# Performance work log

Hardware: AMD Instinct MI355X
Metric: run time of the kernel (lower is better)

## Reference

```python
import jax, jax.numpy as jnp
import numpy as np

B, S, HID = 2, 2048, 2048
H, K, D = 32, 8, 64          # query heads, kv heads, head_dim
G = H // K                   # GQA group size
ROPE_MSCALE = 1.2            # constant rope_mscale applied to q and k
SM_SCALE = 1.0 / (D ** 0.5)  # flash_attn default softmax scale


def rotate_half(x):
    h = x.shape[-1] // 2
    return jnp.concatenate([-x[..., h:], x[..., :h]], axis=-1)


def setup_inputs() -> dict:
    key = jax.random.key(0)
    k1, k2, k3, k4 = jax.random.split(key, 4)
    hidden_states = jax.random.normal(k1, (B, S, HID), dtype=jnp.float32)
    # standard rotary tables: cos/sin of shape [S, D]
    inv_freq = 1.0 / (10000.0 ** (jnp.arange(0, D, 2, dtype=jnp.float32) / D))
    freqs = jnp.outer(jnp.arange(S, dtype=jnp.float32), inv_freq)  # [S, D/2]
    emb = jnp.concatenate([freqs, freqs], axis=-1)                 # [S, D]
    cos, sin = jnp.cos(emb), jnp.sin(emb)
    per_head_scale = 1.0 + 0.1 * jax.random.normal(k2, (B, H), dtype=jnp.float32)
    Wqkv = jax.random.normal(k3, ((H + 2 * K) * D, HID), dtype=jnp.float32) * (HID ** -0.5)
    Wo = jax.random.normal(k4, (HID, H * D), dtype=jnp.float32) * ((H * D) ** -0.5)
    return {"cos": cos, "sin": sin, "hidden_states": hidden_states,
            "per_head_scale": per_head_scale, "Wqkv": Wqkv, "Wo": Wo}


def reference(cos, sin, hidden_states, per_head_scale, Wqkv, Wo):
    # fused QKV projection (CastedLinear, no bias)
    qkv = jnp.einsum('bsh,oh->bso', hidden_states, Wqkv)          # [B,S,(H+2K)*D]
    qkv = qkv.reshape(B, S, H + 2 * K, D)
    q = qkv[:, :, :H]                 # [B,S,H,D]
    k = qkv[:, :, H:H + K]            # [B,S,K,D]
    v = qkv[:, :, H + K:]             # [B,S,K,D]
    # rotary embedding: cos/sin [S,D] -> broadcast over heads via [S,1,D]
    c = cos[:, None, :]
    s_ = sin[:, None, :]
    q = q * c + rotate_half(q) * s_
    k = k * c + rotate_half(k) * s_
    # rope_mscale
    q = q * ROPE_MSCALE
    k = k * ROPE_MSCALE
    # per-head scale on queries: [B,H] -> [B,1,H,1]
    q = q * per_head_scale[:, None, :, None]
    # GQA attention without materializing repeated K/V: group query heads
    qg = q.reshape(B, S, K, G, D)
    scores = jnp.einsum('bqkgd,bskd->bkgqs', qg, k) * SM_SCALE    # [B,K,G,Sq,Sk]
    causal = jnp.arange(S)[:, None] >= jnp.arange(S)[None, :]     # [Sq,Sk]
    scores = jnp.where(causal, scores, jnp.finfo(scores.dtype).min)
    probs = jax.nn.softmax(scores, axis=-1)
    out = jnp.einsum('bkgqs,bskd->bqkgd', probs, v).reshape(B, S, H * D)
    return jnp.einsum('bso,ho->bsh', out, Wo)                     # o_proj
```

## Files before the change

kernel.cpp:

```cpp
#include <hip/hip_runtime.h>
#include <stdint.h>

typedef unsigned short u16;
typedef short short8 __attribute__((ext_vector_type(8)));
typedef float f32x4 __attribute__((ext_vector_type(4)));
typedef uint32_t u32x4 __attribute__((ext_vector_type(4)));

#define S_LEN 2048
#define NQH 32
#define NKH 8
#define DHD 64
#define MNEG -1.0e30f

__device__ __forceinline__ float b2f(u16 u){
  union { uint32_t i; float f; } c; c.i = ((uint32_t)u) << 16; return c.f;
}
__device__ __forceinline__ u16 f2b(float f){
  union { float f; uint32_t i; } c; c.f = f;
  uint32_t r = c.i + 0x7fffu + ((c.i >> 16) & 1u);
  return (u16)(r >> 16);
}
__device__ __forceinline__ uint32_t cvt_pk_bf16(float lo, float hi){
  uint32_t r;
  asm("v_cvt_pk_bf16_f32 %0, %1, %2" : "=v"(r) : "v"(lo), "v"(hi));
  return r;
}
__device__ __forceinline__ void gload_lds16(const void* g, void* l){
  __builtin_amdgcn_global_load_lds((const __attribute__((address_space(1))) uint32_t*)g,
                                   (__attribute__((address_space(3))) uint32_t*)l, 16, 0, 0);
}

__global__ __launch_bounds__(256) void cvt_all(const float* __restrict__ hs,
                                               const float* __restrict__ wq,
                                               const float* __restrict__ wo,
                                               u16* __restrict__ hsB,
                                               u16* __restrict__ wqB,
                                               u16* __restrict__ woB){
  int i = blockIdx.x * 256 + threadIdx.x;
  const float* src; u16* dst; int off;
  if (i < 2097152)      { src = hs; dst = hsB; off = i; }
  else if (i < 3670016) { src = wq; dst = wqB; off = i - 2097152; }
  else                  { src = wo; dst = woB; off = i - 3670016; }
  float4 v = ((const float4*)src)[off];
  uint2 o;
  o.x = (uint32_t)f2b(v.x) | ((uint32_t)f2b(v.y) << 16);
  o.y = (uint32_t)f2b(v.z) | ((uint32_t)f2b(v.w) << 16);
  ((uint2*)dst)[off] = o;
}

template<int OUT_F32>
__global__ __launch_bounds__(256)
void gemm_bt(const u16* __restrict__ A, const u16* __restrict__ Bm,
             void* __restrict__ Cp, int N, int K)
{
  __shared__ alignas(16) u16 lA[128 * 64];
  __shared__ alignas(16) u16 lB[128 * 64];
  const int tid = threadIdx.x;
  const int w = tid >> 6, l = tid & 63;
  const int lg = l >> 4, lc = l & 15;
  const int wm = w >> 1, wn = w & 1;
  const int m0 = blockIdx.y * 128, n0 = blockIdx.x * 128;
  const int srow = l >> 3, sc = l & 7;
  const size_t ldb = (size_t)K * 2;
  f32x4 acc[4][4] = {};
  const int kiters = K >> 6;
  for (int kt = 0; kt < kiters; ++kt){
    __syncthreads();
#pragma unroll
    for (int i = 0; i < 4; ++i){
      const int row = (i * 4 + w) * 8 + srow;
      const int gc = ((sc ^ (row & 7)) << 4);
      gload_lds16((const char*)A + (size_t)(m0 + row) * ldb + (size_t)kt * 128 + gc,
                  (char*)lA + row * 128 + sc * 16);
    }
#pragma unroll
    for (int i = 0; i < 4; ++i){
      const int row = (i * 4 + w) * 8 + srow;
      const int gc = ((sc ^ (row & 7)) << 4);
      gload_lds16((const char*)Bm + (size_t)(n0 + row) * ldb + (size_t)kt * 128 + gc,
                  (char*)lB + row * 128 + sc * 16);
    }
    __syncthreads();
#pragma unroll
    for (int kk = 0; kk < 2; ++kk){
      short8 af[4], bfr[4];
#pragma unroll
      for (int mi = 0; mi < 4; ++mi){
        const int row = wm * 64 + mi * 16 + lc;
        const int cc = (kk * 4 + lg) ^ (row & 7);
        af[mi] = *(const short8*)((const char*)lA + row * 128 + cc * 16);
      }
#pragma unroll
      for (int ni = 0; ni < 4; ++ni){
        const int row = wn * 64 + ni * 16 + lc;
        const int cc = (kk * 4 + lg) ^ (row & 7);
        bfr[ni] = *(const short8*)((const char*)lB + row * 128 + cc * 16);
      }
#pragma unroll
      for (int mi = 0; mi < 4; ++mi)
#pragma unroll
        for (int ni = 0; ni < 4; ++ni)
          acc[mi][ni] = __builtin_amdgcn_mfma_f32_16x16x32_bf16(af[mi], bfr[ni], acc[mi][ni], 0, 0, 0);
    }
  }
  const int r0 = m0 + wm * 64 + lg * 4;
  const int c0 = n0 + wn * 64 + lc;
#pragma unroll
  for (int mi = 0; mi < 4; ++mi)
#pragma unroll
    for (int ni = 0; ni < 4; ++ni)
#pragma unroll
      for (int j = 0; j < 4; ++j){
        const size_t idx = (size_t)(r0 + mi * 16 + j) * (size_t)N + (size_t)(c0 + ni * 16);
        if (OUT_F32) ((float*)Cp)[idx] = acc[mi][ni][j];
        else         ((u16*)Cp)[idx]  = f2b(acc[mi][ni][j]);
      }
}

__global__ __launch_bounds__(256)
void rope_kernel(const u16* __restrict__ qkv, const float* __restrict__ cosT,
                 const float* __restrict__ sinT, const float* __restrict__ phs,
                 u16* __restrict__ Qo, u16* __restrict__ Ko)
{
  int id = blockIdx.x * 256 + threadIdx.x;
  int b = (id >= 327680) ? 1 : 0;
  int rem = id - b * 327680;
  int head = rem >> 13;
  int s = (rem >> 2) & 2047;
  int d0 = (rem & 3) << 4;
  const u16* src = qkv + (((size_t)(b * S_LEN + s) * 48 + head) << 6);
  uint4 xa = *(const uint4*)(src + d0);
  uint4 xb = *(const uint4*)(src + d0 + 8);
  int d0p = (d0 + 32) & 63;
  uint4 pa = *(const uint4*)(src + d0p);
  uint4 pb = *(const uint4*)(src + d0p + 8);
  const float* cp = cosT + s * 64 + d0;
  const float* sp = sinT + s * 64 + d0;
  const float sgn = (d0 < 32) ? -1.f : 1.f;
  const float kscale = 0.18033688011112042f;
  const float scale = (head < NQH) ? 1.2f * kscale * phs[b * NQH + head] : 1.2f;
  uint32_t xs[4] = {xa.x, xa.y, xa.z, xa.w};
  uint32_t xs2[4] = {xb.x, xb.y, xb.z, xb.w};
  uint32_t ps[4] = {pa.x, pa.y, pa.z, pa.w};
  uint32_t ps2[4] = {pb.x, pb.y, pb.z, pb.w};
  uint32_t ow[8];
#pragma unroll
  for (int k = 0; k < 4; ++k){
    float v0 = b2f((u16)(xs[k] & 0xffff)) * cp[2*k]   + sgn * b2f((u16)(ps[k] & 0xffff)) * sp[2*k];
    float v1 = b2f((u16)(xs[k] >> 16))    * cp[2*k+1] + sgn * b2f((u16)(ps[k] >> 16))    * sp[2*k+1];
    ow[k] = (uint32_t)f2b(v0 * scale) | ((uint32_t)f2b(v1 * scale) << 16);
  }
#pragma unroll
  for (int k = 0; k < 4; ++k){
    float v0 = b2f((u16)(xs2[k] & 0xffff)) * cp[8+2*k]   + sgn * b2f((u16)(ps2[k] & 0xffff)) * sp[8+2*k];
    float v1 = b2f((u16)(xs2[k] >> 16))    * cp[8+2*k+1] + sgn * b2f((u16)(ps2[k] >> 16))    * sp[8+2*k+1];
    ow[4+k] = (uint32_t)f2b(v0 * scale) | ((uint32_t)f2b(v1 * scale) << 16);
  }
  u16* dst;
  if (head < NQH) dst = Qo + (((size_t)(b * NQH + head) * S_LEN + s) << 6) + d0;
  else            dst = Ko + (((size_t)(b * NKH + head - NQH) * S_LEN + s) << 6) + d0;
  uint4 o0 = {ow[0], ow[1], ow[2], ow[3]};
  uint4 o1 = {ow[4], ow[5], ow[6], ow[7]};
  *(uint4*)dst = o0;
  *(uint4*)(dst + 8) = o1;
}

__global__ __launch_bounds__(256)
void vtrans(const u16* __restrict__ qkv, u16* __restrict__ VT)
{
  int bid = blockIdx.x;
  int t = bid & 15, kh = (bid >> 4) & 7, b = bid >> 7;
  __shared__ u16 vlds[128][72];
  int tid = threadIdx.x;
  {
    int r = tid >> 1, half = tid & 1;
    const u16* src = qkv + (((size_t)(b * S_LEN + t * 128 + r) * 48 + 40 + kh) << 6) + half * 32;
    uint4 a0 = *(const uint4*)(src);
    uint4 a1 = *(const uint4*)(src + 8);
    uint4 a2 = *(const uint4*)(src + 16);
    uint4 a3 = *(const uint4*)(src + 24);
    *(uint4*)&vlds[r][half * 32]      = a0;
    *(uint4*)&vlds[r][half * 32 + 8]  = a1;
    *(uint4*)&vlds[r][half * 32 + 16] = a2;
    *(uint4*)&vlds[r][half * 32 + 24] = a3;
  }
  __syncthreads();
  const int d = tid >> 2, kk2 = tid & 3;
  u16* dst = VT + ((size_t)(b * NKH + kh) * 64 + d) * S_LEN + t * 128 + kk2 * 32;
#pragma unroll
  for (int j = 0; j < 4; ++j){
    u16 o[8];
#pragma unroll
    for (int e = 0; e < 8; ++e){
      const int hk = kk2 * 32 + ((e >> 2) << 4) + j * 4 + (e & 3);
      o[e] = vlds[hk][d];
    }
    uint4 ov = { (uint32_t)o[0] | ((uint32_t)o[1] << 16), (uint32_t)o[2] | ((uint32_t)o[3] << 16),
                 (uint32_t)o[4] | ((uint32_t)o[5] << 16), (uint32_t)o[6] | ((uint32_t)o[7] << 16) };
    *(uint4*)(dst + j * 8) = ov;
  }
}

__device__ __forceinline__ void proc_chunk(f32x4 (&sv)[8], float& mrow, float& lsum,
                                           f32x4 (&o)[4], uint32_t (&pw)[4][4],
                                           const int lg, const int lc,
                                           const bool diag, const int qloc)
{
  if (diag){
#pragma unroll
    for (int nj = 0; nj < 8; ++nj)
#pragma unroll
      for (int jj = 0; jj < 4; ++jj){
        const int kloc = nj * 16 + lg * 4 + jj;
        if (kloc > qloc) sv[nj][jj] = MNEG;
      }
  }
  float mu = sv[0][0];
#pragma unroll
  for (int nj = 0; nj < 8; ++nj)
#pragma unroll
    for (int jj = 0; jj < 4; ++jj) mu = fmaxf(mu, sv[nj][jj]);
  mu = fmaxf(mu, __shfl_xor(mu, 16));
  mu = fmaxf(mu, __shfl_xor(mu, 32));
  if (!__all(mu <= mrow + 11.54f)){
    const float mnew = fmaxf(mrow, mu);
    const float sf = __builtin_amdgcn_exp2f(mrow - mnew);
    mrow = mnew;
    lsum *= sf;
#pragma unroll
    for (int dn = 0; dn < 4; ++dn)
#pragma unroll
      for (int jj = 0; jj < 4; ++jj) o[dn][jj] *= sf;
  }
  const float mcur = mrow;
  float ps = 0.f;
#pragma unroll
  for (int nj = 0; nj < 8; ++nj)
#pragma unroll
    for (int jj = 0; jj < 4; ++jj){
      const float pv = __builtin_amdgcn_exp2f(sv[nj][jj] - mcur);
      sv[nj][jj] = pv;
      ps += pv;
    }
  lsum += ps;
#pragma unroll
  for (int kk2 = 0; kk2 < 4; ++kk2){
    pw[kk2][0] = cvt_pk_bf16(sv[kk2 * 2][0],     sv[kk2 * 2][1]);
    pw[kk2][1] = cvt_pk_bf16(sv[kk2 * 2][2],     sv[kk2 * 2][3]);
    pw[kk2][2] = cvt_pk_bf16(sv[kk2 * 2 + 1][0], sv[kk2 * 2 + 1][1]);
    pw[kk2][3] = cvt_pk_bf16(sv[kk2 * 2 + 1][2], sv[kk2 * 2 + 1][3]);
  }
}

__device__ __forceinline__ short8 pw_frag(const uint32_t* pw){
  u32x4 v = { pw[0], pw[1], pw[2], pw[3] };
  return __builtin_bit_cast(short8, v);
}

__global__ __launch_bounds__(512, 2)
void attn_kernel(const u16* __restrict__ Q, const u16* __restrict__ Kr,
                 const u16* __restrict__ VT, u16* __restrict__ Ao)
{
  int bid = blockIdx.x;
  int p  = bid & 15;
  int gp = (bid >> 4) & 1;
  int kh = (bid >> 5) & 7;
  int b  = bid >> 8;
  const int qt0 = p, qt1 = 31 - p;

  __shared__ alignas(16) u16 lK[2][128 * 64];
  __shared__ alignas(16) u16 lV[2][64 * 128];

  const int tid = threadIdx.x;
  const int hh = tid >> 8;
  const int h  = kh * 4 + gp * 2 + hh;
  const int w  = (tid >> 6) & 3;
  const int l  = tid & 63;
  const int lg = l >> 4, lc = l & 15;

  short8 qf[2][2];
  {
    const u16* qbase = Q + ((size_t)(b * NQH + h) * S_LEN) * 64;
#pragma unroll
    for (int kk = 0; kk < 2; ++kk){
      qf[0][kk] = *(const short8*)(qbase + (size_t)(qt0 * 64 + w * 16 + lc) * 64 + kk * 32 + lg * 8);
      qf[1][kk] = *(const short8*)(qbase + (size_t)(qt1 * 64 + w * 16 + lc) * 64 + kk * 32 + lg * 8);
    }
  }

  const u16* Kb = Kr + (size_t)(b * NKH + kh) * S_LEN * 64;
  const u16* Vb = VT + (size_t)(b * NKH + kh) * 64 * S_LEN;

  f32x4 o[2][4] = {};
  float mrow[2] = {MNEG, MNEG};
  float lsum[2] = {0.f, 0.f};

  const int nt = (qt1 >> 1) + 1;
  const int nt0 = qt0 >> 1;

#define STAGE(T, BSEL) do { \
    _Pragma("unroll") \
    for (int i_ = 0; i_ < 2; ++i_){ \
      const int row_ = i_ * 64 + (tid >> 3); \
      const int ch_  = tid & 7; \
      const int gc_  = ((ch_ ^ (row_ & 7)) << 4); \
      gload_lds16((const char*)(Kb + (size_t)((T) * 128 + row_) * 64) + gc_, \
                  (char*)lK[BSEL] + row_ * 128 + ch_ * 16); \
    } \
    _Pragma("unroll") \
    for (int i_ = 0; i_ < 2; ++i_){ \
      const int row_ = i_ * 32 + (tid >> 4); \
      const int ch_  = tid & 15; \
      const int gc_  = ((ch_ ^ (row_ & 15)) << 4); \
      gload_lds16((const char*)(Vb + (size_t)row_ * S_LEN + (T) * 128) + gc_, \
                  (char*)lV[BSEL] + row_ * 256 + ch_ * 16); \
    } \
  } while (0)

  STAGE(0, 0);

  for (int t = 0; t < nt; ++t){
    const int cur = t & 1;
    const bool act0 = (t <= nt0);
    if (t + 1 < nt){
      STAGE(t + 1, cur ^ 1);
      asm volatile("s_waitcnt vmcnt(4)" ::: "memory");
    } else {
      asm volatile("s_waitcnt vmcnt(0)" ::: "memory");
    }
    __builtin_amdgcn_s_barrier();

    f32x4 sv[2][8] = {};
    __builtin_amdgcn_s_setprio(1);
#pragma unroll
    for (int kk = 0; kk < 2; ++kk){
      short8 kf[8];
#pragma unroll
      for (int nj = 0; nj < 8; ++nj){
        const int row = nj * 16 + lc;
        const int cc = (kk * 4 + lg) ^ (row & 7);
        kf[nj] = *(const short8*)((const char*)lK[cur] + row * 128 + cc * 16);
      }
      if (act0)
#pragma unroll
        for (int nj = 0; nj < 8; ++nj)
          sv[0][nj] = __builtin_amdgcn_mfma_f32_16x16x32_bf16(kf[nj], qf[0][kk], sv[0][nj], 0, 0, 0);
#pragma unroll
      for (int nj = 0; nj < 8; ++nj)
        sv[1][nj] = __builtin_amdgcn_mfma_f32_16x16x32_bf16(kf[nj], qf[1][kk], sv[1][nj], 0, 0, 0);
    }
    __builtin_amdgcn_s_setprio(0);

    uint32_t pw[2][4][4];
    if (act0)
      proc_chunk(sv[0], mrow[0], lsum[0], o[0], pw[0], lg, lc,
                 t == (qt0 >> 1), (qt0 & 1) * 64 + w * 16 + lc);
    proc_chunk(sv[1], mrow[1], lsum[1], o[1], pw[1], lg, lc,
               t == (qt1 >> 1), (qt1 & 1) * 64 + w * 16 + lc);

    __builtin_amdgcn_s_setprio(1);
#pragma unroll
    for (int kk2 = 0; kk2 < 4; ++kk2){
      short8 vf[4];
#pragma unroll
      for (int dn = 0; dn < 4; ++dn){
        const int row = dn * 16 + lc;
        const int cc = (kk2 * 4 + lg) ^ (row & 15);
        vf[dn] = *(const short8*)((const char*)lV[cur] + row * 256 + cc * 16);
      }
      if (act0){
        const short8 pb0 = pw_frag(pw[0][kk2]);
#pragma unroll
        for (int dn = 0; dn < 4; ++dn)
          o[0][dn] = __builtin_amdgcn_mfma_f32_16x16x32_bf16(vf[dn], pb0, o[0][dn], 0, 0, 0);
      }
      const short8 pb1 = pw_frag(pw[1][kk2]);
#pragma unroll
      for (int dn = 0; dn < 4; ++dn)
        o[1][dn] = __builtin_amdgcn_mfma_f32_16x16x32_bf16(vf[dn], pb1, o[1][dn], 0, 0, 0);
    }
    __builtin_amdgcn_s_setprio(0);
    __builtin_amdgcn_s_barrier();
  }
#undef STAGE

#pragma unroll
  for (int c = 0; c < 2; ++c){
    const int qt = c ? qt1 : qt0;
    float ls = lsum[c];
    ls += __shfl_xor(ls, 16);
    ls += __shfl_xor(ls, 32);
    const float inv = 1.f / ls;
    const int sq = qt * 64 + w * 16 + lc;
#pragma unroll
    for (int dn = 0; dn < 4; ++dn){
      uint2 pk;
      pk.x = cvt_pk_bf16(o[c][dn][0] * inv, o[c][dn][1] * inv);
      pk.y = cvt_pk_bf16(o[c][dn][2] * inv, o[c][dn][3] * inv);
      const int col = h * 64 + dn * 16 + lg * 4;
      *(uint2*)&Ao[(size_t)(b * S_LEN + sq) * 2048 + col] = pk;
    }
  }
}

extern "C" void kernel_launch(void* const* d_in, const int* in_sizes, int n_in,
                              void* d_out, int out_size, void* d_ws, size_t ws_size,
                              hipStream_t stream)
{
  const float* cosT = (const float*)d_in[0];
  const float* sinT = (const float*)d_in[1];
  const float* hs   = (const float*)d_in[2];
  const float* phs  = (const float*)d_in[3];
  const float* Wqkv = (const float*)d_in[4];
  const float* Wo   = (const float*)d_in[5];
  float* out = (float*)d_out;
  char* ws = (char*)d_ws;

  u16* hsB   = (u16*)(ws);
  u16* WqkvB = (u16*)(ws + 16777216);
  u16* WoB   = (u16*)(ws + 29360128);
  u16* qkvB  = (u16*)(ws + 37748736);
  u16* Qb    = (u16*)(ws + 62914560);
  u16* Kb    = (u16*)(ws + 79691776);
  u16* VTb   = (u16*)(ws + 83886080);
  u16* Ao    = hsB;

  cvt_all<<<18432, 256, 0, stream>>>(hs, Wqkv, Wo, hsB, WqkvB, WoB);
  gemm_bt<0><<<dim3(24, 32), 256, 0, stream>>>(hsB, WqkvB, (void*)qkvB, 3072, 2048);
  rope_kernel<<<2560, 256, 0, stream>>>(qkvB, cosT, sinT, phs, Qb, Kb);
  vtrans<<<256, 256, 0, stream>>>(qkvB, VTb);
  attn_kernel<<<512, 512, 0, stream>>>(Qb, Kb, VTb, Ao);
  gemm_bt<1><<<dim3(16, 32), 256, 0, stream>>>(Ao, WoB, (void*)out, 2048, 2048);
}
```

Before: 223.7 us.

## Split each KV tile across two half-blocks and merge partial softmax states

The attention kernel now gives each block one query head instead of two. The two 256-thread halves each process 64 of the 128 keys in every staged KV tile, which doubles the grid to 1024 blocks. Each half keeps its own online-softmax state, and at the end the partial outputs, row maxes and sums are merged through shared memory, flash-decoding style. A half also skips its work on diagonal tiles that are fully masked. The intent is more parallelism and shorter per-block latency, at the cost of loading each K/V tile twice as often across blocks, plus an extra LDS merge and more syncs.

```diff
diff --git a/kernel.cpp b/kernel.cpp
--- a/kernel.cpp
+++ b/kernel.cpp
@@ -201,23 +201,23 @@
   }
 }
 
-__device__ __forceinline__ void proc_chunk(f32x4 (&sv)[8], float& mrow, float& lsum,
-                                           f32x4 (&o)[4], uint32_t (&pw)[4][4],
-                                           const int lg, const int lc,
-                                           const bool diag, const int qloc)
+__device__ __forceinline__ void proc_chunk4(f32x4 (&sv)[4], float& mrow, float& lsum,
+                                            f32x4 (&o)[4], uint32_t (&pw)[2][4],
+                                            const int lg, const int lc,
+                                            const bool diag, const int qloc, const int kvbase)
 {
   if (diag){
 #pragma unroll
-    for (int nj = 0; nj < 8; ++nj)
+    for (int nj = 0; nj < 4; ++nj)
 #pragma unroll
       for (int jj = 0; jj < 4; ++jj){
-        const int kloc = nj * 16 + lg * 4 + jj;
+        const int kloc = kvbase + nj * 16 + lg * 4 + jj;
         if (kloc > qloc) sv[nj][jj] = MNEG;
       }
   }
   float mu = sv[0][0];
 #pragma unroll
-  for (int nj = 0; nj < 8; ++nj)
+  for (int nj = 0; nj < 4; ++nj)
 #pragma unroll
     for (int jj = 0; jj < 4; ++jj) mu = fmaxf(mu, sv[nj][jj]);
   mu = fmaxf(mu, __shfl_xor(mu, 16));
@@ -235,7 +235,7 @@
   const float mcur = mrow;
   float ps = 0.f;
 #pragma unroll
-  for (int nj = 0; nj < 8; ++nj)
+  for (int nj = 0; nj < 4; ++nj)
 #pragma unroll
     for (int jj = 0; jj < 4; ++jj){
       const float pv = __builtin_amdgcn_exp2f(sv[nj][jj] - mcur);
@@ -244,11 +244,11 @@
     }
   lsum += ps;
 #pragma unroll
-  for (int kk2 = 0; kk2 < 4; ++kk2){
-    pw[kk2][0] = cvt_pk_bf16(sv[kk2 * 2][0],     sv[kk2 * 2][1]);
-    pw[kk2][1] = cvt_pk_bf16(sv[kk2 * 2][2],     sv[kk2 * 2][3]);
-    pw[kk2][2] = cvt_pk_bf16(sv[kk2 * 2 + 1][0], sv[kk2 * 2 + 1][1]);
-    pw[kk2][3] = cvt_pk_bf16(sv[kk2 * 2 + 1][2], sv[kk2 * 2 + 1][3]);
+  for (int k2 = 0; k2 < 2; ++k2){
+    pw[k2][0] = cvt_pk_bf16(sv[k2 * 2][0],     sv[k2 * 2][1]);
+    pw[k2][1] = cvt_pk_bf16(sv[k2 * 2][2],     sv[k2 * 2][3]);
+    pw[k2][2] = cvt_pk_bf16(sv[k2 * 2 + 1][0], sv[k2 * 2 + 1][1]);
+    pw[k2][3] = cvt_pk_bf16(sv[k2 * 2 + 1][2], sv[k2 * 2 + 1][3]);
   }
 }
 
@@ -263,20 +263,22 @@
 {
   int bid = blockIdx.x;
   int p  = bid & 15;
-  int gp = (bid >> 4) & 1;
-  int kh = (bid >> 5) & 7;
-  int b  = bid >> 8;
+  int g  = (bid >> 4) & 3;
+  int kh = (bid >> 6) & 7;
+  int b  = bid >> 9;
+  const int h = kh * 4 + g;
   const int qt0 = p, qt1 = 31 - p;
 
-  __shared__ alignas(16) u16 lK[2][128 * 64];
-  __shared__ alignas(16) u16 lV[2][64 * 128];
+  __shared__ alignas(16) u16 smem[32768];
+  char* lKb = (char*)smem;
+  char* lVb = (char*)smem + 32768;
 
   const int tid = threadIdx.x;
-  const int hh = tid >> 8;
-  const int h  = kh * 4 + gp * 2 + hh;
-  const int w  = (tid >> 6) & 3;
-  const int l  = tid & 63;
+  const int kvg = tid >> 8;
+  const int w   = (tid >> 6) & 3;
+  const int l   = tid & 63;
   const int lg = l >> 4, lc = l & 15;
+  const int kvbase = kvg * 64;
 
   short8 qf[2][2];
   {
@@ -295,8 +297,10 @@
   float mrow[2] = {MNEG, MNEG};
   float lsum[2] = {0.f, 0.f};
 
-  const int nt = (qt1 >> 1) + 1;
+  const int nt  = (qt1 >> 1) + 1;
   const int nt0 = qt0 >> 1;
+  const int td0 = qt0 >> 1, td1 = qt1 >> 1;
+  const bool odd0 = (qt0 & 1) != 0, odd1 = (qt1 & 1) != 0;
 
 #define STAGE(T, BSEL) do { \
     _Pragma("unroll") \
@@ -305,7 +309,7 @@
       const int ch_  = tid & 7; \
       const int gc_  = ((ch_ ^ (row_ & 7)) << 4); \
       gload_lds16((const char*)(Kb + (size_t)((T) * 128 + row_) * 64) + gc_, \
-                  (char*)lK[BSEL] + row_ * 128 + ch_ * 16); \
+                  lKb + (BSEL) * 16384 + row_ * 128 + ch_ * 16); \
     } \
     _Pragma("unroll") \
     for (int i_ = 0; i_ < 2; ++i_){ \
@@ -313,7 +317,7 @@
       const int ch_  = tid & 15; \
       const int gc_  = ((ch_ ^ (row_ & 15)) << 4); \
       gload_lds16((const char*)(Vb + (size_t)row_ * S_LEN + (T) * 128) + gc_, \
-                  (char*)lV[BSEL] + row_ * 256 + ch_ * 16); \
+                  lVb + (BSEL) * 16384 + row_ * 256 + ch_ * 16); \
     } \
   } while (0)
 
@@ -321,7 +325,8 @@
 
   for (int t = 0; t < nt; ++t){
     const int cur = t & 1;
-    const bool act0 = (t <= nt0);
+    const bool a0 = (t <= nt0) && !(kvg == 1 && t == td0 && !odd0);
+    const bool a1 = !(kvg == 1 && t == td1 && !odd1);
     if (t + 1 < nt){
       STAGE(t + 1, cur ^ 1);
       asm volatile("s_waitcnt vmcnt(4)" ::: "memory");
@@ -330,75 +335,112 @@
     }
     __builtin_amdgcn_s_barrier();
 
-    f32x4 sv[2][8] = {};
+    f32x4 sv[2][4] = {};
     __builtin_amdgcn_s_setprio(1);
 #pragma unroll
     for (int kk = 0; kk < 2; ++kk){
-      short8 kf[8];
-#pragma unroll
-      for (int nj = 0; nj < 8; ++nj){
-        const int row = nj * 16 + lc;
+      short8 kf[4];
+#pragma unroll
+      for (int nj = 0; nj < 4; ++nj){
+        const int row = kvbase + nj * 16 + lc;
         const int cc = (kk * 4 + lg) ^ (row & 7);
-        kf[nj] = *(const short8*)((const char*)lK[cur] + row * 128 + cc * 16);
-      }
-      if (act0)
-#pragma unroll
-        for (int nj = 0; nj < 8; ++nj)
+        kf[nj] = *(const short8*)(lKb + cur * 16384 + row * 128 + cc * 16);
+      }
+      if (a0)
+#pragma unroll
+        for (int nj = 0; nj < 4; ++nj)
           sv[0][nj] = __builtin_amdgcn_mfma_f32_16x16x32_bf16(kf[nj], qf[0][kk], sv[0][nj], 0, 0, 0);
-#pragma unroll
-      for (int nj = 0; nj < 8; ++nj)
-        sv[1][nj] = __builtin_amdgcn_mfma_f32_16x16x32_bf16(kf[nj], qf[1][kk], sv[1][nj], 0, 0, 0);
+      if (a1)
+#pragma unroll
+        for (int nj = 0; nj < 4; ++nj)
+          sv[1][nj] = __builtin_amdgcn_mfma_f32_16x16x32_bf16(kf[nj], qf[1][kk], sv[1][nj], 0, 0, 0);
     }
     __builtin_amdgcn_s_setprio(0);
 
-    uint32_t pw[2][4][4];
-    if (act0)
-      proc_chunk(sv[0], mrow[0], lsum[0], o[0], pw[0], lg, lc,
-                 t == (qt0 >> 1), (qt0 & 1) * 64 + w * 16 + lc);
-    proc_chunk(sv[1], mrow[1], lsum[1], o[1], pw[1], lg, lc,
-               t == (qt1 >> 1), (qt1 & 1) * 64 + w * 16 + lc);
+    uint32_t pw[2][2][4];
+    if (a0)
+      proc_chunk4(sv[0], mrow[0], lsum[0], o[0], pw[0], lg, lc,
+                  t == td0, (qt0 & 1) * 64 + w * 16 + lc, kvbase);
+    if (a1)
+      proc_chunk4(sv[1], mrow[1], lsum[1], o[1], pw[1], lg, lc,
+                  t == td1, (qt1 & 1) * 64 + w * 16 + lc, kvbase);
 
     __builtin_amdgcn_s_setprio(1);
 #pragma unroll
-    for (int kk2 = 0; kk2 < 4; ++kk2){
+    for (int k2 = 0; k2 < 2; ++k2){
+      const int kk2g = kvg * 2 + k2;
       short8 vf[4];
 #pragma unroll
       for (int dn = 0; dn < 4; ++dn){
         const int row = dn * 16 + lc;
-        const int cc = (kk2 * 4 + lg) ^ (row & 15);
-        vf[dn] = *(const short8*)((const char*)lV[cur] + row * 256 + cc * 16);
-      }
-      if (act0){
-        const short8 pb0 = pw_frag(pw[0][kk2]);
+        const int cc = (kk2g * 4 + lg) ^ (row & 15);
+        vf[dn] = *(const short8*)(lVb + cur * 16384 + row * 256 + cc * 16);
+      }
+      if (a0){
+        const short8 pb0 = pw_frag(pw[0][k2]);
 #pragma unroll
         for (int dn = 0; dn < 4; ++dn)
           o[0][dn] = __builtin_amdgcn_mfma_f32_16x16x32_bf16(vf[dn], pb0, o[0][dn], 0, 0, 0);
       }
-      const short8 pb1 = pw_frag(pw[1][kk2]);
-#pragma unroll
-      for (int dn = 0; dn < 4; ++dn)
-        o[1][dn] = __builtin_amdgcn_mfma_f32_16x16x32_bf16(vf[dn], pb1, o[1][dn], 0, 0, 0);
+      if (a1){
+        const short8 pb1 = pw_frag(pw[1][k2]);
+#pragma unroll
+        for (int dn = 0; dn < 4; ++dn)
+          o[1][dn] = __builtin_amdgcn_mfma_f32_16x16x32_bf16(vf[dn], pb1, o[1][dn], 0, 0, 0);
+      }
     }
     __builtin_amdgcn_s_setprio(0);
     __builtin_amdgcn_s_barrier();
   }
 #undef STAGE
 
+  float ls[2];
 #pragma unroll
   for (int c = 0; c < 2; ++c){
-    const int qt = c ? qt1 : qt0;
-    float ls = lsum[c];
-    ls += __shfl_xor(ls, 16);
-    ls += __shfl_xor(ls, 32);
-    const float inv = 1.f / ls;
-    const int sq = qt * 64 + w * 16 + lc;
-#pragma unroll
-    for (int dn = 0; dn < 4; ++dn){
-      uint2 pk;
-      pk.x = cvt_pk_bf16(o[c][dn][0] * inv, o[c][dn][1] * inv);
-      pk.y = cvt_pk_bf16(o[c][dn][2] * inv, o[c][dn][3] * inv);
-      const int col = h * 64 + dn * 16 + lg * 4;
-      *(uint2*)&Ao[(size_t)(b * S_LEN + sq) * 2048 + col] = pk;
+    float v = lsum[c];
+    v += __shfl_xor(v, 16);
+    v += __shfl_xor(v, 32);
+    ls[c] = v;
+  }
+  __syncthreads();
+  float* mb = (float*)smem;
+  if (kvg == 1){
+#pragma unroll
+    for (int c = 0; c < 2; ++c){
+      float* base = mb + (((w * 2 + c) * 64) + l) * 20;
+#pragma unroll
+      for (int dn = 0; dn < 4; ++dn)
+        *(f32x4*)(base + dn * 4) = o[c][dn];
+      base[16] = mrow[c];
+      base[17] = ls[c];
+    }
+  }
+  __syncthreads();
+  if (kvg == 0){
+#pragma unroll
+    for (int c = 0; c < 2; ++c){
+      const int qt = c ? qt1 : qt0;
+      float* base = mb + (((w * 2 + c) * 64) + l) * 20;
+      const float mB = base[16];
+      const float lB = base[17];
+      const float m  = fmaxf(mrow[c], mB);
+      const float wA = __builtin_amdgcn_exp2f(mrow[c] - m);
+      const float wB = __builtin_amdgcn_exp2f(mB - m);
+      const float inv = 1.f / (ls[c] * wA + lB * wB);
+      const int sq = qt * 64 + w * 16 + lc;
+#pragma unroll
+      for (int dn = 0; dn < 4; ++dn){
+        f32x4 ob = *(const f32x4*)(base + dn * 4);
+        float v0 = (o[c][dn][0] * wA + ob[0] * wB) * inv;
+        float v1 = (o[c][dn][1] * wA + ob[1] * wB) * inv;
+        float v2 = (o[c][dn][2] * wA + ob[2] * wB) * inv;
+        float v3 = (o[c][dn][3] * wA + ob[3] * wB) * inv;
+        uint2 pk;
+        pk.x = cvt_pk_bf16(v0, v1);
+        pk.y = cvt_pk_bf16(v2, v3);
+        const int col = h * 64 + dn * 16 + lg * 4;
+        *(uint2*)&Ao[(size_t)(b * S_LEN + sq) * 2048 + col] = pk;
+      }
     }
   }
 }
@@ -429,6 +471,6 @@
   gemm_bt<0><<<dim3(24, 32), 256, 0, stream>>>(hsB, WqkvB, (void*)qkvB, 3072, 2048);
   rope_kernel<<<2560, 256, 0, stream>>>(qkvB, cosT, sinT, phs, Qb, Kb);
   vtrans<<<256, 256, 0, stream>>>(qkvB, VTb);
-  attn_kernel<<<512, 512, 0, stream>>>(Qb, Kb, VTb, Ao);
+  attn_kernel<<<1024, 512, 0, stream>>>(Qb, Kb, VTb, Ao);
   gemm_bt<1><<<dim3(16, 32), 256, 0, stream>>>(Ao, WoB, (void*)out, 2048, 2048);
 }
```

Result: slower. 235.5 us (+5.3%).

## Fuse RoPE and Q/K scaling into QKV GEMM epilogue, pack cos/sin as bf16

Applied to the files above, without the earlier changes.

Removes the standalone rope kernel by applying rotary embedding, mscale and per-head scale directly on the QKV GEMM accumulators, writing Q and K in head-major layout and raw V to a compact buffer. cos/sin tables are packed to bf16 pairs inside the conversion kernel. This avoids writing and rereading the full qkv intermediate and drops a launch. The trade-offs are scattered 2-byte stores in the epilogue and rounding cos/sin to bf16.

```diff
diff --git a/kernel.cpp b/kernel.cpp
--- a/kernel.cpp
+++ b/kernel.cpp
@@ -33,10 +33,24 @@
 __global__ __launch_bounds__(256) void cvt_all(const float* __restrict__ hs,
                                                const float* __restrict__ wq,
                                                const float* __restrict__ wo,
+                                               const float* __restrict__ cosp,
+                                               const float* __restrict__ sinp,
                                                u16* __restrict__ hsB,
                                                u16* __restrict__ wqB,
-                                               u16* __restrict__ woB){
+                                               u16* __restrict__ woB,
+                                               uint32_t* __restrict__ csB){
   int i = blockIdx.x * 256 + threadIdx.x;
+  if (i >= 4718592){
+    int off = i - 4718592;
+    float4 c = ((const float4*)cosp)[off];
+    float4 s = ((const float4*)sinp)[off];
+    u32x4 o = { (uint32_t)f2b(c.x) | ((uint32_t)f2b(s.x) << 16),
+                (uint32_t)f2b(c.y) | ((uint32_t)f2b(s.y) << 16),
+                (uint32_t)f2b(c.z) | ((uint32_t)f2b(s.z) << 16),
+                (uint32_t)f2b(c.w) | ((uint32_t)f2b(s.w) << 16) };
+    ((u32x4*)csB)[off] = o;
+    return;
+  }
   const float* src; u16* dst; int off;
   if (i < 2097152)      { src = hs; dst = hsB; off = i; }
   else if (i < 3670016) { src = wq; dst = wqB; off = i - 2097152; }
@@ -118,55 +132,101 @@
 }
 
 __global__ __launch_bounds__(256)
-void rope_kernel(const u16* __restrict__ qkv, const float* __restrict__ cosT,
-                 const float* __restrict__ sinT, const float* __restrict__ phs,
-                 u16* __restrict__ Qo, u16* __restrict__ Ko)
-{
-  int id = blockIdx.x * 256 + threadIdx.x;
-  int b = (id >= 327680) ? 1 : 0;
-  int rem = id - b * 327680;
-  int head = rem >> 13;
-  int s = (rem >> 2) & 2047;
-  int d0 = (rem & 3) << 4;
-  const u16* src = qkv + (((size_t)(b * S_LEN + s) * 48 + head) << 6);
-  uint4 xa = *(const uint4*)(src + d0);
-  uint4 xb = *(const uint4*)(src + d0 + 8);
-  int d0p = (d0 + 32) & 63;
-  uint4 pa = *(const uint4*)(src + d0p);
-  uint4 pb = *(const uint4*)(src + d0p + 8);
-  const float* cp = cosT + s * 64 + d0;
-  const float* sp = sinT + s * 64 + d0;
-  const float sgn = (d0 < 32) ? -1.f : 1.f;
-  const float kscale = 0.18033688011112042f;
-  const float scale = (head < NQH) ? 1.2f * kscale * phs[b * NQH + head] : 1.2f;
-  uint32_t xs[4] = {xa.x, xa.y, xa.z, xa.w};
-  uint32_t xs2[4] = {xb.x, xb.y, xb.z, xb.w};
-  uint32_t ps[4] = {pa.x, pa.y, pa.z, pa.w};
-  uint32_t ps2[4] = {pb.x, pb.y, pb.z, pb.w};
-  uint32_t ow[8];
-#pragma unroll
-  for (int k = 0; k < 4; ++k){
-    float v0 = b2f((u16)(xs[k] & 0xffff)) * cp[2*k]   + sgn * b2f((u16)(ps[k] & 0xffff)) * sp[2*k];
-    float v1 = b2f((u16)(xs[k] >> 16))    * cp[2*k+1] + sgn * b2f((u16)(ps[k] >> 16))    * sp[2*k+1];
-    ow[k] = (uint32_t)f2b(v0 * scale) | ((uint32_t)f2b(v1 * scale) << 16);
-  }
-#pragma unroll
-  for (int k = 0; k < 4; ++k){
-    float v0 = b2f((u16)(xs2[k] & 0xffff)) * cp[8+2*k]   + sgn * b2f((u16)(ps2[k] & 0xffff)) * sp[8+2*k];
-    float v1 = b2f((u16)(xs2[k] >> 16))    * cp[8+2*k+1] + sgn * b2f((u16)(ps2[k] >> 16))    * sp[8+2*k+1];
-    ow[4+k] = (uint32_t)f2b(v0 * scale) | ((uint32_t)f2b(v1 * scale) << 16);
-  }
-  u16* dst;
-  if (head < NQH) dst = Qo + (((size_t)(b * NQH + head) * S_LEN + s) << 6) + d0;
-  else            dst = Ko + (((size_t)(b * NKH + head - NQH) * S_LEN + s) << 6) + d0;
-  uint4 o0 = {ow[0], ow[1], ow[2], ow[3]};
-  uint4 o1 = {ow[4], ow[5], ow[6], ow[7]};
-  *(uint4*)dst = o0;
-  *(uint4*)(dst + 8) = o1;
+void gemm1_rope(const u16* __restrict__ A, const u16* __restrict__ Bm,
+                const uint32_t* __restrict__ cs, const float* __restrict__ phs,
+                u16* __restrict__ Qo, u16* __restrict__ Ko, u16* __restrict__ Vraw)
+{
+  __shared__ alignas(16) u16 lA[128 * 64];
+  __shared__ alignas(16) u16 lB[128 * 64];
+  const int tid = threadIdx.x;
+  const int w = tid >> 6, l = tid & 63;
+  const int lg = l >> 4, lc = l & 15;
+  const int wm = w >> 1, wn = w & 1;
+  const int m0 = blockIdx.y * 128, n0 = blockIdx.x * 128;
+  const int srow = l >> 3, sc = l & 7;
+  const size_t ldb = 4096;
+  f32x4 acc[4][4] = {};
+  for (int kt = 0; kt < 32; ++kt){
+    __syncthreads();
+#pragma unroll
+    for (int i = 0; i < 4; ++i){
+      const int row = (i * 4 + w) * 8 + srow;
+      const int gc = ((sc ^ (row & 7)) << 4);
+      gload_lds16((const char*)A + (size_t)(m0 + row) * ldb + (size_t)kt * 128 + gc,
+                  (char*)lA + row * 128 + sc * 16);
+    }
+#pragma unroll
+    for (int i = 0; i < 4; ++i){
+      const int row = (i * 4 + w) * 8 + srow;
+      const int gc = ((sc ^ (row & 7)) << 4);
+      gload_lds16((const char*)Bm + (size_t)(n0 + row) * ldb + (size_t)kt * 128 + gc,
+                  (char*)lB + row * 128 + sc * 16);
+    }
+    __syncthreads();
+#pragma unroll
+    for (int kk = 0; kk < 2; ++kk){
+      short8 af[4], bfr[4];
+#pragma unroll
+      for (int mi = 0; mi < 4; ++mi){
+        const int row = wm * 64 + mi * 16 + lc;
+        const int cc = (kk * 4 + lg) ^ (row & 7);
+        af[mi] = *(const short8*)((const char*)lA + row * 128 + cc * 16);
+      }
+#pragma unroll
+      for (int ni = 0; ni < 4; ++ni){
+        const int row = wn * 64 + ni * 16 + lc;
+        const int cc = (kk * 4 + lg) ^ (row & 7);
+        bfr[ni] = *(const short8*)((const char*)lB + row * 128 + cc * 16);
+      }
+#pragma unroll
+      for (int mi = 0; mi < 4; ++mi)
+#pragma unroll
+        for (int ni = 0; ni < 4; ++ni)
+          acc[mi][ni] = __builtin_amdgcn_mfma_f32_16x16x32_bf16(af[mi], bfr[ni], acc[mi][ni], 0, 0, 0);
+    }
+  }
+  const int r0 = m0 + wm * 64 + lg * 4;
+  const int c0 = n0 + wn * 64 + lc;
+  const int head = (n0 + wn * 64) >> 6;
+  const int b = m0 >> 11;
+  if (head < 40){
+    const float scale = (head < NQH) ? 1.2f * 0.18033688011112042f * phs[b * NQH + head] : 1.2f;
+    u16* dstbase = (head < NQH)
+        ? (Qo + ((size_t)(b * NQH + head) * S_LEN) * 64)
+        : (Ko + ((size_t)(b * NKH + (head - NQH)) * S_LEN) * 64);
+#pragma unroll
+    for (int mi = 0; mi < 4; ++mi)
+#pragma unroll
+      for (int j = 0; j < 4; ++j){
+        const int s = (r0 + mi * 16 + j) & 2047;
+        const uint32_t* csrow = cs + s * 64;
+        float xs[4] = {acc[mi][0][j], acc[mi][1][j], acc[mi][2][j], acc[mi][3][j]};
+#pragma unroll
+        for (int ni = 0; ni < 4; ++ni){
+          const int d = lc + ni * 16;
+          const uint32_t csv = csrow[d];
+          const float cv = b2f((u16)(csv & 0xffff));
+          const float sv = b2f((u16)(csv >> 16));
+          const float sgn = (ni < 2) ? -1.f : 1.f;
+          const float v = (xs[ni] * cv + sgn * xs[ni ^ 2] * sv) * scale;
+          dstbase[(size_t)s * 64 + d] = f2b(v);
+        }
+      }
+  } else {
+#pragma unroll
+    for (int mi = 0; mi < 4; ++mi)
+#pragma unroll
+      for (int ni = 0; ni < 4; ++ni)
+#pragma unroll
+        for (int j = 0; j < 4; ++j){
+          const int r = r0 + mi * 16 + j;
+          Vraw[(size_t)r * 512 + (c0 + ni * 16 - 2560)] = f2b(acc[mi][ni][j]);
+        }
+  }
 }
 
 __global__ __launch_bounds__(256)
-void vtrans(const u16* __restrict__ qkv, u16* __restrict__ VT)
+void vtrans(const u16* __restrict__ Vraw, u16* __restrict__ VT)
 {
   int bid = blockIdx.x;
   int t = bid & 15, kh = (bid >> 4) & 7, b = bid >> 7;
@@ -174,7 +234,7 @@
   int tid = threadIdx.x;
   {
     int r = tid >> 1, half = tid & 1;
-    const u16* src = qkv + (((size_t)(b * S_LEN + t * 128 + r) * 48 + 40 + kh) << 6) + half * 32;
+    const u16* src = Vraw + (((size_t)(b * S_LEN + t * 128 + r) * 8 + kh) << 6) + half * 32;
     uint4 a0 = *(const uint4*)(src);
     uint4 a1 = *(const uint4*)(src + 8);
     uint4 a2 = *(const uint4*)(src + 16);
@@ -419,16 +479,16 @@
   u16* hsB   = (u16*)(ws);
   u16* WqkvB = (u16*)(ws + 16777216);
   u16* WoB   = (u16*)(ws + 29360128);
-  u16* qkvB  = (u16*)(ws + 37748736);
-  u16* Qb    = (u16*)(ws + 62914560);
-  u16* Kb    = (u16*)(ws + 79691776);
-  u16* VTb   = (u16*)(ws + 83886080);
+  u16* Vraw  = (u16*)(ws + 37748736);
+  u16* Qb    = (u16*)(ws + 41943040);
+  u16* Kb    = (u16*)(ws + 58720256);
+  u16* VTb   = (u16*)(ws + 62914560);
+  uint32_t* csB = (uint32_t*)(ws + 67108864);
   u16* Ao    = hsB;
 
-  cvt_all<<<18432, 256, 0, stream>>>(hs, Wqkv, Wo, hsB, WqkvB, WoB);
-  gemm_bt<0><<<dim3(24, 32), 256, 0, stream>>>(hsB, WqkvB, (void*)qkvB, 3072, 2048);
-  rope_kernel<<<2560, 256, 0, stream>>>(qkvB, cosT, sinT, phs, Qb, Kb);
-  vtrans<<<256, 256, 0, stream>>>(qkvB, VTb);
+  cvt_all<<<18560, 256, 0, stream>>>(hs, Wqkv, Wo, cosT, sinT, hsB, WqkvB, WoB, csB);
+  gemm1_rope<<<dim3(24, 32), 256, 0, stream>>>(hsB, WqkvB, csB, phs, Qb, Kb, Vraw);
+  vtrans<<<256, 256, 0, stream>>>(Vraw, VTb);
   attn_kernel<<<512, 512, 0, stream>>>(Qb, Kb, VTb, Ao);
   gemm_bt<1><<<dim3(16, 32), 256, 0, stream>>>(Ao, WoB, (void*)out, 2048, 2048);
 }
```

Result: no change. 224.8 us (+0.5%).
